# Optimization experiments

Measured on AMD Instinct MI355X. Metric: run time of the kernel, lower is better.

The kernel has to match this reference:

```python
import jax, jax.numpy as jnp
import numpy as np


def setup_inputs() -> dict:
    key = jax.random.key(0)
    ks = jax.random.split(key, 11)
    B, E, R, D = 2048, 20000, 500, 256
    inp = {
        "h": jax.random.uniform(ks[0], (B, E), dtype=jnp.float32),
        "t": jax.random.uniform(ks[1], (B, E), dtype=jnp.float32),
        "r": jax.random.uniform(ks[2], (B, R), dtype=jnp.float32),
        "W_er": jax.random.normal(ks[3], (D, E), dtype=jnp.float32) * 0.02,
        "W_ei": jax.random.normal(ks[4], (D, E), dtype=jnp.float32) * 0.02,
        "W_ej": jax.random.normal(ks[5], (D, E), dtype=jnp.float32) * 0.02,
        "W_ek": jax.random.normal(ks[6], (D, E), dtype=jnp.float32) * 0.02,
        "W_rr": jax.random.normal(ks[7], (D, R), dtype=jnp.float32) * 0.02,
        "W_ri": jax.random.normal(ks[8], (D, R), dtype=jnp.float32) * 0.02,
        "W_rj": jax.random.normal(ks[9], (D, R), dtype=jnp.float32) * 0.02,
        "W_rk": jax.random.normal(ks[10], (D, R), dtype=jnp.float32) * 0.02,
    }
    return inp


def reference(h, t, r, W_er, W_ei, W_ej, W_ek, W_rr, W_ri, W_rj, W_rk):
    # entity / relation projections (nn.Linear, no bias): x @ W^T -> [B, D]
    H_r, H_i, H_j, H_k = h @ W_er.T, h @ W_ei.T, h @ W_ej.T, h @ W_ek.T
    T_r, T_i, T_j, T_k = t @ W_er.T, t @ W_ei.T, t @ W_ej.T, t @ W_ek.T
    R_r, R_i, R_j, R_k = r @ W_rr.T, r @ W_ri.T, r @ W_rj.T, r @ W_rk.T

    # hypercomplex norm per row: sqrt(|R_r|^2 + |R_i|^2 + |R_j|^2 + |R_k|^2) -> [B,1]
    norm = jnp.sqrt(
        jnp.sum(R_r * R_r + R_i * R_i + R_j * R_j + R_k * R_k, axis=1, keepdims=True)
    )
    R_r, R_i, R_j, R_k = norm * R_r, norm * R_i, norm * R_j, norm * R_k

    # Hamilton product H (x) R
    Q_r = H_r * R_r - H_i * R_i - H_j * R_j - H_k * R_k
    Q_i = H_r * R_i + H_i * R_r + H_j * R_k - H_k * R_j
    Q_j = H_r * R_j - H_i * R_k + H_j * R_r + H_k * R_i
    Q_k = H_r * R_k + H_i * R_j - H_j * R_i + H_k * R_r

    # diag(Q @ T^T) == rowwise dot sum(Q*T, axis=1) -- O(B*d) form of the anti-pattern
    score = jnp.sum(Q_r * T_r + Q_i * T_i + Q_j * T_j + Q_k * T_k, axis=1, keepdims=True)
    return jax.nn.sigmoid(score)
```

## Files before the change

### kernel.cpp

```cpp
#include <hip/hip_runtime.h>


using bf16x8 = __attribute__((ext_vector_type(8))) short;
using f32x4  = __attribute__((ext_vector_type(4))) float;

#define DEVINL static __device__ __forceinline__

DEVINL void split2(float x0, float x1, unsigned& h, unsigned& l) {
  unsigned u0 = __float_as_uint(x0), u1 = __float_as_uint(x1);
  unsigned h0 = u0 & 0xFFFF0000u, h1 = u1 & 0xFFFF0000u;
  h = (u0 >> 16) | h1;
  float r0 = x0 - __uint_as_float(h0);
  float r1 = x1 - __uint_as_float(h1);
  l = (__float_as_uint(r0) >> 16) | (__float_as_uint(r1) & 0xFFFF0000u);
}

DEVINL void gload16(const void* g, void* l) {
  __builtin_amdgcn_global_load_lds(
      (const __attribute__((address_space(1))) unsigned*)g,
      (__attribute__((address_space(3))) unsigned*)l, 16, 0, 0);
}

__global__ void convert_b(const float* __restrict__ src, int srcK,
                          char* __restrict__ dst)
{
  const int tile = blockIdx.x;
  const int wrow = threadIdx.x;
  char* base = dst + (size_t)tile * 32768;
  const float* srow = src + (size_t)wrow * srcK;
#pragma unroll
  for (int kc8 = 0; kc8 < 4; ++kc8) {
    int k0 = tile * 32 + kc8 * 8;
    float x[8];
    if (k0 + 8 <= srcK) {
      float4 v0 = *(const float4*)(srow + k0);
      float4 v1 = *(const float4*)(srow + k0 + 4);
      x[0] = v0.x; x[1] = v0.y; x[2] = v0.z; x[3] = v0.w;
      x[4] = v1.x; x[5] = v1.y; x[6] = v1.z; x[7] = v1.w;
    } else {
#pragma unroll
      for (int j = 0; j < 8; ++j) x[j] = (k0 + j < srcK) ? srow[k0 + j] : 0.f;
    }
    unsigned hh[4], ll[4];
    split2(x[0], x[1], hh[0], ll[0]);
    split2(x[2], x[3], hh[1], ll[1]);
    split2(x[4], x[5], hh[2], ll[2]);
    split2(x[6], x[7], hh[3], ll[3]);
    int lchunk = (wrow & 15) + kc8 * 16;
    int n16 = wrow >> 4;
    *(uint4*)(base + (size_t)n16 * 1024 + lchunk * 16)         = make_uint4(hh[0], hh[1], hh[2], hh[3]);
    *(uint4*)(base + 16384 + (size_t)n16 * 1024 + lchunk * 16) = make_uint4(ll[0], ll[1], ll[2], ll[3]);
  }
}

__global__ void pad_r(const float* __restrict__ src, float* __restrict__ dst)
{
  int row = blockIdx.y;
  int c4 = threadIdx.x;
  int k = c4 * 4;
  float4 v = make_float4(0.f, 0.f, 0.f, 0.f);
  if (k + 3 < 500) v = *(const float4*)(src + (size_t)row * 500 + k);
  *(float4*)(dst + (size_t)row * 512 + k) = v;
}

__global__ __launch_bounds__(512, 2) void gemm3p(
    const float* __restrict__ A0, const float* __restrict__ A1, int mtA0, long lda,
    const char* __restrict__ Bimg, int ktilesTot,
    float* __restrict__ C, long ldc, int MT, int NT, int KS, int swz)
{
  extern __shared__ char smem[];
  const int tid = threadIdx.x;
  const int bid = blockIdx.x;

  int mt, nt, ks;
  if (swz) {
    int x = bid & 7, w = bid >> 3;
    nt = w & 3;
    int g = x + (w >> 2) * 8;
    mt = g & 15; ks = g >> 4;
  } else {
    nt = bid % NT; int q = bid / NT; mt = q % MT; ks = q / MT;
  }

  const int kt0 = (ktilesTot * ks) / KS;
  const int kt1 = (ktilesTot * (ks + 1)) / KS;

  const float* Ablk = (mt < mtA0) ? (A0 + (size_t)mt * 256 * lda)
                                  : (A1 + (size_t)(mt - mtA0) * 256 * lda);
  const char* Bt = Bimg + ((size_t)nt * ktilesTot + kt0) * 32768;

  const int wid = tid >> 6, lane = tid & 63;
  const int wr = wid >> 2, wc = wid & 3;
  const int l15 = lane & 15, lq = lane >> 4;

  const float* aSrc = Ablk + (size_t)(wid * 32 + (lane >> 3)) * lda
                      + (size_t)kt0 * 32 + 4 * (lane & 7);

  int awoff[4];
  {
    int kg = (lane & 7) >> 1, half = lane & 1;
#pragma unroll
    for (int i = 0; i < 4; ++i) {
      int m15 = (lane >> 3) + 8 * (i & 1);
      awoff[i] = (2 * wid + (i >> 1)) * 2048 + (((m15 ^ kg) + kg * 16) << 4) + half * 8;
    }
  }
  const int aroff = (((l15 ^ lq) + lq * 16) << 4);
  const int bbase = 32768 + (wc * 4) * 1024 + lane * 16;

  f32x4 acc[8][4];
#pragma unroll
  for (int m = 0; m < 8; ++m)
#pragma unroll
    for (int j = 0; j < 4; ++j)
#pragma unroll
      for (int e = 0; e < 4; ++e) acc[m][j][e] = 0.f;

  float4 aR[4];

#define ISSUE_A(KT)                                                            \
  {                                                                            \
    const float* p_ = aSrc + (size_t)((KT) - kt0) * 32;                        \
    _Pragma("unroll")                                                          \
    for (int i = 0; i < 4; ++i) aR[i] = *(const float4*)(p_ + (size_t)(8 * i) * lda); \
  }
#define ISSUE_B(DST, KT)                                                       \
  {                                                                            \
    const char* p_ = Bt + (size_t)((KT) - kt0) * 32768 + wid * 4096 + lane * 16; \
    _Pragma("unroll")                                                          \
    for (int i = 0; i < 4; ++i)                                                \
      gload16(p_ + i * 1024, (DST) + 32768 + wid * 4096 + i * 1024);           \
  }
#define WRITE_A(DST)                                                           \
  {                                                                            \
    _Pragma("unroll")                                                          \
    for (int i = 0; i < 4; ++i) {                                              \
      unsigned h0_, l0_, h1_, l1_;                                             \
      split2(aR[i].x, aR[i].y, h0_, l0_);                                      \
      split2(aR[i].z, aR[i].w, h1_, l1_);                                      \
      *(uint2*)((DST) + awoff[i])        = make_uint2(h0_, h1_);               \
      *(uint2*)((DST) + awoff[i] + 1024) = make_uint2(l0_, l1_);               \
    }                                                                          \
  }

  ISSUE_A(kt0);
  ISSUE_B(smem, kt0);
  WRITE_A(smem);
  asm volatile("s_waitcnt vmcnt(0)" ::: "memory");
  asm volatile("s_waitcnt lgkmcnt(0)" ::: "memory");
  __builtin_amdgcn_s_barrier();

  for (int kt = kt0; kt < kt1; ++kt) {
    char* bufc = smem + (size_t)((kt - kt0) & 1) * 65536;
    char* bufn = smem + (size_t)(((kt - kt0) & 1) ^ 1) * 65536;
    const bool nx = (kt + 1 < kt1);

    if (nx) { ISSUE_A(kt + 1); ISSUE_B(bufn, kt + 1); }

    bf16x8 bh[4], bl[4];
#pragma unroll
    for (int j = 0; j < 4; ++j) {
      bh[j] = *(const bf16x8*)(bufc + bbase + j * 1024);
      bl[j] = *(const bf16x8*)(bufc + bbase + j * 1024 + 16384);
    }

    __builtin_amdgcn_s_setprio(1);
#pragma unroll
    for (int m = 0; m < 4; ++m) {
      const char* ab = bufc + (wr * 8 + m) * 2048;
      bf16x8 ah = *(const bf16x8*)(ab + aroff);
      bf16x8 al = *(const bf16x8*)(ab + aroff + 1024);
#pragma unroll
      for (int j = 0; j < 4; ++j) {
        acc[m][j] = __builtin_amdgcn_mfma_f32_16x16x32_bf16(ah, bh[j], acc[m][j], 0, 0, 0);
        acc[m][j] = __builtin_amdgcn_mfma_f32_16x16x32_bf16(al, bh[j], acc[m][j], 0, 0, 0);
        acc[m][j] = __builtin_amdgcn_mfma_f32_16x16x32_bf16(ah, bl[j], acc[m][j], 0, 0, 0);
      }
    }
    __builtin_amdgcn_s_setprio(0);

    __builtin_amdgcn_sched_barrier(0);
    if (nx) WRITE_A(bufn);

    __builtin_amdgcn_s_setprio(1);
#pragma unroll
    for (int m = 4; m < 8; ++m) {
      const char* ab = bufc + (wr * 8 + m) * 2048;
      bf16x8 ah = *(const bf16x8*)(ab + aroff);
      bf16x8 al = *(const bf16x8*)(ab + aroff + 1024);
#pragma unroll
      for (int j = 0; j < 4; ++j) {
        acc[m][j] = __builtin_amdgcn_mfma_f32_16x16x32_bf16(ah, bh[j], acc[m][j], 0, 0, 0);
        acc[m][j] = __builtin_amdgcn_mfma_f32_16x16x32_bf16(al, bh[j], acc[m][j], 0, 0, 0);
        acc[m][j] = __builtin_amdgcn_mfma_f32_16x16x32_bf16(ah, bl[j], acc[m][j], 0, 0, 0);
      }
    }
    __builtin_amdgcn_s_setprio(0);

    asm volatile("s_waitcnt vmcnt(0)" ::: "memory");
    asm volatile("s_waitcnt lgkmcnt(0)" ::: "memory");
    __builtin_amdgcn_s_barrier();
  }
#undef ISSUE_A
#undef ISSUE_B
#undef WRITE_A

  float* Cb = C + (size_t)ks * (size_t)(MT * 256) * (size_t)ldc;
  const long rowbase = (long)mt * 256 + wr * 128 + lq * 4;
  const long colbase = (long)nt * 256 + wc * 64 + l15;
#pragma unroll
  for (int m = 0; m < 8; ++m)
#pragma unroll
    for (int j = 0; j < 4; ++j)
#pragma unroll
      for (int reg = 0; reg < 4; ++reg) {
        long row = rowbase + m * 16 + reg;
        long col = colbase + j * 16;
        Cb[(size_t)row * ldc + col] = acc[m][j][reg];
      }
}

__global__ void epilogue_kernel(const float* __restrict__ C1, const float* __restrict__ C2,
                                float* __restrict__ out, int KS)
{
  const int b = blockIdx.x;
  const int d = threadIdx.x;
  const size_t SZ = 4096ull * 1024ull;

  float Hq[4], Tq[4], Rq[4];
#pragma unroll
  for (int q = 0; q < 4; ++q) {
    float hv = 0.f, tv = 0.f;
    for (int ks = 0; ks < KS; ++ks) {
      hv += C1[ks * SZ + (size_t)b * 1024 + q * 256 + d];
      tv += C1[ks * SZ + (size_t)(b + 2048) * 1024 + q * 256 + d];
    }
    Hq[q] = hv; Tq[q] = tv;
    Rq[q] = C2[(size_t)b * 1024 + q * 256 + d];
  }
  float nn = Rq[0]*Rq[0] + Rq[1]*Rq[1] + Rq[2]*Rq[2] + Rq[3]*Rq[3];
  float Qr = Hq[0]*Rq[0] - Hq[1]*Rq[1] - Hq[2]*Rq[2] - Hq[3]*Rq[3];
  float Qi = Hq[0]*Rq[1] + Hq[1]*Rq[0] + Hq[2]*Rq[3] - Hq[3]*Rq[2];
  float Qj = Hq[0]*Rq[2] - Hq[1]*Rq[3] + Hq[2]*Rq[0] + Hq[3]*Rq[1];
  float Qk = Hq[0]*Rq[3] + Hq[1]*Rq[2] - Hq[2]*Rq[1] + Hq[3]*Rq[0];
  float ss = Qr*Tq[0] + Qi*Tq[1] + Qj*Tq[2] + Qk*Tq[3];

#pragma unroll
  for (int o = 32; o; o >>= 1) {
    ss += __shfl_xor(ss, o);
    nn += __shfl_xor(nn, o);
  }
  __shared__ float red[8];
  int lane = d & 63, w = d >> 6;
  if (lane == 0) { red[w] = ss; red[4 + w] = nn; }
  __syncthreads();
  if (d == 0) {
    float S = red[0] + red[1] + red[2] + red[3];
    float N = red[4] + red[5] + red[6] + red[7];
    float score = sqrtf(N) * S;
    out[b] = 1.f / (1.f + expf(-score));
  }
}

extern "C" void kernel_launch(void* const* d_in, const int* in_sizes, int n_in,
                              void* d_out, int out_size, void* d_ws, size_t ws_size,
                              hipStream_t stream)
{
  const float* h = (const float*)d_in[0];
  const float* t = (const float*)d_in[1];
  const float* r = (const float*)d_in[2];
  const float* We[4] = {(const float*)d_in[3], (const float*)d_in[4],
                        (const float*)d_in[5], (const float*)d_in[6]};
  const float* Wr[4] = {(const float*)d_in[7], (const float*)d_in[8],
                        (const float*)d_in[9], (const float*)d_in[10]};
  float* out = (float*)d_out;

  char* ws = (char*)d_ws;
  const size_t offB  = 0;
  const size_t offWr = 81920000;
  const size_t offR  = offWr + 2097152;
  const size_t offC1 = offR + 4194304;
  const size_t C1sz  = 4096ull * 1024ull * 4ull;
  const int KS = (ws_size >= offC1 + 4 * C1sz + 8388608ull) ? 4 : 2;
  const size_t offC2 = offC1 + (size_t)KS * C1sz;

  float* rpad = (float*)(ws + offR);
  float* C1   = (float*)(ws + offC1);
  float* C2   = (float*)(ws + offC2);

  for (int q = 0; q < 4; ++q) {
    convert_b<<<dim3(625), 256, 0, stream>>>(We[q], 20000, ws + offB + (size_t)q * 625 * 32768);
    convert_b<<<dim3(16), 256, 0, stream>>>(Wr[q], 500, ws + offWr + (size_t)q * 16 * 32768);
  }
  pad_r<<<dim3(1, 2048), 128, 0, stream>>>(r, rpad);

  gemm3p<<<dim3(16 * 4 * KS), 512, 131072, stream>>>(
      h, t, 8, 20000L, (const char*)(ws + offB), 625,
      C1, 1024L, 16, 4, KS, KS == 4 ? 1 : 0);
  gemm3p<<<dim3(32), 512, 131072, stream>>>(
      rpad, rpad, 8, 512L, (const char*)(ws + offWr), 16,
      C2, 1024L, 8, 4, 1, 0);

  epilogue_kernel<<<dim3(2048), 256, 0, stream>>>(C1, C2, out, KS);
}
```

Before: 687.2 us.

## Split GEMM main loop into four barrier-synchronized LDS-read/MFMA phases

The per-k-tile inner loop is restructured into four phases, each reading A fragments for two m-rows from LDS and then running their MFMAs, with workgroup barriers between phases. All waves thereby alternate LDS-read and MFMA bursts in lockstep, aiming to cut LDS contention and overlap the global prefetch with compute. The extra barriers add synchronization overhead and can stall waves that would otherwise run ahead, and the final lgkmcnt wait before the loop-end barrier is removed.

```diff
diff --git a/kernel.cpp b/kernel.cpp
--- a/kernel.cpp
+++ b/kernel.cpp
@@ -142,6 +142,33 @@
       *(uint2*)((DST) + awoff[i] + 1024) = make_uint2(l0_, l1_);               \
     }                                                                          \
   }
+#define MFMA_PAIR(M0)                                                          \
+  {                                                                            \
+    _Pragma("unroll")                                                          \
+    for (int mm = 0; mm < 2; ++mm) {                                           \
+      bf16x8 ah = a_h[mm], al = a_l[mm];                                       \
+      _Pragma("unroll")                                                        \
+      for (int j = 0; j < 4; ++j) {                                            \
+        f32x4* a = &acc[(M0) + mm][j];                                         \
+        *a = __builtin_amdgcn_mfma_f32_16x16x32_bf16(ah, bh[j], *a, 0, 0, 0);  \
+        *a = __builtin_amdgcn_mfma_f32_16x16x32_bf16(al, bh[j], *a, 0, 0, 0);  \
+        *a = __builtin_amdgcn_mfma_f32_16x16x32_bf16(ah, bl[j], *a, 0, 0, 0);  \
+      }                                                                        \
+    }                                                                          \
+  }
+#define READ_A_PAIR(M0)                                                        \
+  {                                                                            \
+    _Pragma("unroll")                                                          \
+    for (int mm = 0; mm < 2; ++mm) {                                           \
+      const char* ab_ = abase + ((M0) + mm) * 2048;                            \
+      a_h[mm] = *(const bf16x8*)(ab_ + aroff);                                 \
+      a_l[mm] = *(const bf16x8*)(ab_ + aroff + 1024);                          \
+    }                                                                          \
+  }
+#define PHASE_SYNC()                                                           \
+  __builtin_amdgcn_s_barrier();                                                \
+  asm volatile("s_waitcnt lgkmcnt(0)" ::: "memory");                           \
+  __builtin_amdgcn_sched_barrier(0);
 
   ISSUE_A(kt0);
   ISSUE_B(smem, kt0);
@@ -154,56 +181,52 @@
     char* bufc = smem + (size_t)((kt - kt0) & 1) * 65536;
     char* bufn = smem + (size_t)(((kt - kt0) & 1) ^ 1) * 65536;
     const bool nx = (kt + 1 < kt1);
+    const char* abase = bufc + wr * 8 * 2048;
+
+    bf16x8 bh[4], bl[4], a_h[2], a_l[2];
 
     if (nx) { ISSUE_A(kt + 1); ISSUE_B(bufn, kt + 1); }
-
-    bf16x8 bh[4], bl[4];
 #pragma unroll
     for (int j = 0; j < 4; ++j) {
       bh[j] = *(const bf16x8*)(bufc + bbase + j * 1024);
       bl[j] = *(const bf16x8*)(bufc + bbase + j * 1024 + 16384);
     }
-
+    READ_A_PAIR(0);
+    PHASE_SYNC();
     __builtin_amdgcn_s_setprio(1);
-#pragma unroll
-    for (int m = 0; m < 4; ++m) {
-      const char* ab = bufc + (wr * 8 + m) * 2048;
-      bf16x8 ah = *(const bf16x8*)(ab + aroff);
-      bf16x8 al = *(const bf16x8*)(ab + aroff + 1024);
-#pragma unroll
-      for (int j = 0; j < 4; ++j) {
-        acc[m][j] = __builtin_amdgcn_mfma_f32_16x16x32_bf16(ah, bh[j], acc[m][j], 0, 0, 0);
-        acc[m][j] = __builtin_amdgcn_mfma_f32_16x16x32_bf16(al, bh[j], acc[m][j], 0, 0, 0);
-        acc[m][j] = __builtin_amdgcn_mfma_f32_16x16x32_bf16(ah, bl[j], acc[m][j], 0, 0, 0);
-      }
-    }
+    MFMA_PAIR(0);
     __builtin_amdgcn_s_setprio(0);
-
-    __builtin_amdgcn_sched_barrier(0);
+    __builtin_amdgcn_s_barrier();
+
+    READ_A_PAIR(2);
+    PHASE_SYNC();
+    __builtin_amdgcn_s_setprio(1);
+    MFMA_PAIR(2);
+    __builtin_amdgcn_s_setprio(0);
+    __builtin_amdgcn_s_barrier();
+
     if (nx) WRITE_A(bufn);
-
+    READ_A_PAIR(4);
+    PHASE_SYNC();
     __builtin_amdgcn_s_setprio(1);
-#pragma unroll
-    for (int m = 4; m < 8; ++m) {
-      const char* ab = bufc + (wr * 8 + m) * 2048;
-      bf16x8 ah = *(const bf16x8*)(ab + aroff);
-      bf16x8 al = *(const bf16x8*)(ab + aroff + 1024);
-#pragma unroll
-      for (int j = 0; j < 4; ++j) {
-        acc[m][j] = __builtin_amdgcn_mfma_f32_16x16x32_bf16(ah, bh[j], acc[m][j], 0, 0, 0);
-        acc[m][j] = __builtin_amdgcn_mfma_f32_16x16x32_bf16(al, bh[j], acc[m][j], 0, 0, 0);
-        acc[m][j] = __builtin_amdgcn_mfma_f32_16x16x32_bf16(ah, bl[j], acc[m][j], 0, 0, 0);
-      }
-    }
+    MFMA_PAIR(4);
     __builtin_amdgcn_s_setprio(0);
-
+    __builtin_amdgcn_s_barrier();
+
+    READ_A_PAIR(6);
+    PHASE_SYNC();
+    __builtin_amdgcn_s_setprio(1);
+    MFMA_PAIR(6);
+    __builtin_amdgcn_s_setprio(0);
     asm volatile("s_waitcnt vmcnt(0)" ::: "memory");
-    asm volatile("s_waitcnt lgkmcnt(0)" ::: "memory");
     __builtin_amdgcn_s_barrier();
   }
 #undef ISSUE_A
 #undef ISSUE_B
 #undef WRITE_A
+#undef MFMA_PAIR
+#undef READ_A_PAIR
+#undef PHASE_SYNC
 
   float* Cb = C + (size_t)ks * (size_t)(MT * 256) * (size_t)ldc;
   const long rowbase = (long)mt * 256 + wr * 128 + lq * 4;
```

Result: slower. 739.8 us (+7.7%).

## Pre-split activations into bf16 hi/lo tile images and use 32x32 MFMA GEMM

Applied to the files above, without the earlier changes.

Adds a conversion pass that writes h, t and r as pre-split bf16 hi/lo tiled images, so the GEMM loads both operands straight into LDS with global_load_lds instead of splitting A in registers each k-tile. The new GEMM uses 32x32x16 MFMA with a 4x2 block per wave and a static 128KB shared buffer. This removes per-tile VALU splitting and register staging of A, but adds a full extra pass that reads the large activations and writes an image of the same size. The new path runs only when the workspace is large enough, otherwise it falls back to the old kernels.

```diff
diff --git a/kernel.cpp b/kernel.cpp
--- a/kernel.cpp
+++ b/kernel.cpp
@@ -3,6 +3,7 @@
 
 using bf16x8 = __attribute__((ext_vector_type(8))) short;
 using f32x4  = __attribute__((ext_vector_type(4))) float;
+using f32x16 = __attribute__((ext_vector_type(16))) float;
 
 #define DEVINL static __device__ __forceinline__
 
@@ -21,8 +22,153 @@
       (__attribute__((address_space(3))) unsigned*)l, 16, 0, 0);
 }
 
-__global__ void convert_b(const float* __restrict__ src, int srcK,
-                          char* __restrict__ dst)
+__global__ void convert_img(const float* __restrict__ src0,
+                            const float* __restrict__ src1, int rows0,
+                            int srcK, char* __restrict__ dst, int ktiles)
+{
+  const int kt = blockIdx.x, rt = blockIdx.y;
+  const int m  = threadIdx.x;
+  const int row = rt * 256 + m;
+  const float* srow = (row < rows0) ? (src0 + (size_t)row * srcK)
+                                    : (src1 + (size_t)(row - rows0) * srcK);
+  char* base = dst + ((size_t)rt * ktiles + kt) * 32768
+             + (m >> 5) * 2048 + (m & 31) * 16;
+#pragma unroll
+  for (int oct = 0; oct < 4; ++oct) {
+    int k0 = kt * 32 + oct * 8;
+    float x[8];
+    if (k0 + 8 <= srcK) {
+      float4 v0 = *(const float4*)(srow + k0);
+      float4 v1 = *(const float4*)(srow + k0 + 4);
+      x[0] = v0.x; x[1] = v0.y; x[2] = v0.z; x[3] = v0.w;
+      x[4] = v1.x; x[5] = v1.y; x[6] = v1.z; x[7] = v1.w;
+    } else {
+#pragma unroll
+      for (int j = 0; j < 8; ++j) x[j] = (k0 + j < srcK) ? srow[k0 + j] : 0.f;
+    }
+    unsigned hh[4], ll[4];
+    split2(x[0], x[1], hh[0], ll[0]);
+    split2(x[2], x[3], hh[1], ll[1]);
+    split2(x[4], x[5], hh[2], ll[2]);
+    split2(x[6], x[7], hh[3], ll[3]);
+    int off = (oct >> 1) * 1024 + (oct & 1) * 512;
+    *(uint4*)(base + off)         = make_uint4(hh[0], hh[1], hh[2], hh[3]);
+    *(uint4*)(base + 16384 + off) = make_uint4(ll[0], ll[1], ll[2], ll[3]);
+  }
+}
+
+__global__ __launch_bounds__(512, 2) void gemm_img(
+    const char* __restrict__ Aimg, const char* __restrict__ Bimg, int ktiles,
+    float* __restrict__ C, int MT, int NT, int KS, int swz)
+{
+  __shared__ __align__(16) char smem[131072];
+  const int tid = threadIdx.x;
+  const int bid = blockIdx.x;
+
+  int mt, nt, ks;
+  if (swz) {
+    int x = bid & 7, w = bid >> 3;
+    nt = w & 3;
+    int g = x + (w >> 2) * 8;
+    mt = g & 15; ks = g >> 4;
+  } else {
+    nt = bid % NT; int q = bid / NT; mt = q % MT; ks = q / MT;
+  }
+
+  const int kt0 = (ktiles * ks) / KS;
+  const int kt1 = (ktiles * (ks + 1)) / KS;
+
+  const char* Ab = Aimg + ((size_t)mt * ktiles + kt0) * 32768;
+  const char* Bb = Bimg + ((size_t)nt * ktiles + kt0) * 32768;
+
+  const int wid = tid >> 6, lane = tid & 63;
+  const int wr = wid >> 2, wc = wid & 3;
+
+  f32x16 acc[4][2];
+#pragma unroll
+  for (int mb = 0; mb < 4; ++mb)
+#pragma unroll
+    for (int nb = 0; nb < 2; ++nb)
+#pragma unroll
+      for (int e = 0; e < 16; ++e) acc[mb][nb][e] = 0.f;
+
+  {
+    const char* As = Ab + wid * 4096 + lane * 16;
+    const char* Bs = Bb + wid * 4096 + lane * 16;
+#pragma unroll
+    for (int i = 0; i < 4; ++i) gload16(As + i * 1024, smem + wid * 4096 + i * 1024);
+#pragma unroll
+    for (int i = 0; i < 4; ++i) gload16(Bs + i * 1024, smem + 32768 + wid * 4096 + i * 1024);
+  }
+  asm volatile("s_waitcnt vmcnt(0)" ::: "memory");
+  __builtin_amdgcn_s_barrier();
+
+  for (int kt = kt0; kt < kt1; ++kt) {
+    char* bufc = smem + (size_t)((kt - kt0) & 1) * 65536;
+    char* bufn = smem + (size_t)(((kt - kt0) & 1) ^ 1) * 65536;
+    const bool nx = (kt + 1 < kt1);
+
+    if (nx) {
+      const char* As = Ab + (size_t)(kt + 1 - kt0) * 32768 + wid * 4096 + lane * 16;
+      const char* Bs = Bb + (size_t)(kt + 1 - kt0) * 32768 + wid * 4096 + lane * 16;
+#pragma unroll
+      for (int i = 0; i < 4; ++i) gload16(As + i * 1024, bufn + wid * 4096 + i * 1024);
+#pragma unroll
+      for (int i = 0; i < 4; ++i) gload16(Bs + i * 1024, bufn + 32768 + wid * 4096 + i * 1024);
+    }
+
+    bf16x8 bh[2][2], bl[2][2];
+#pragma unroll
+    for (int nb = 0; nb < 2; ++nb)
+#pragma unroll
+      for (int s = 0; s < 2; ++s) {
+        const char* p = bufc + 32768 + (wc * 2 + nb) * 2048 + s * 1024 + lane * 16;
+        bh[nb][s] = *(const bf16x8*)p;
+        bl[nb][s] = *(const bf16x8*)(p + 16384);
+      }
+
+    __builtin_amdgcn_s_setprio(1);
+#pragma unroll
+    for (int mb = 0; mb < 4; ++mb) {
+      const char* p = bufc + (wr * 4 + mb) * 2048 + lane * 16;
+      bf16x8 ah0 = *(const bf16x8*)(p);
+      bf16x8 al0 = *(const bf16x8*)(p + 16384);
+      bf16x8 ah1 = *(const bf16x8*)(p + 1024);
+      bf16x8 al1 = *(const bf16x8*)(p + 1024 + 16384);
+#pragma unroll
+      for (int nb = 0; nb < 2; ++nb) {
+        f32x16* a = &acc[mb][nb];
+        *a = __builtin_amdgcn_mfma_f32_32x32x16_bf16(ah0, bh[nb][0], *a, 0, 0, 0);
+        *a = __builtin_amdgcn_mfma_f32_32x32x16_bf16(al0, bh[nb][0], *a, 0, 0, 0);
+        *a = __builtin_amdgcn_mfma_f32_32x32x16_bf16(ah0, bl[nb][0], *a, 0, 0, 0);
+        *a = __builtin_amdgcn_mfma_f32_32x32x16_bf16(ah1, bh[nb][1], *a, 0, 0, 0);
+        *a = __builtin_amdgcn_mfma_f32_32x32x16_bf16(al1, bh[nb][1], *a, 0, 0, 0);
+        *a = __builtin_amdgcn_mfma_f32_32x32x16_bf16(ah1, bl[nb][1], *a, 0, 0, 0);
+      }
+    }
+    __builtin_amdgcn_s_setprio(0);
+
+    asm volatile("s_waitcnt vmcnt(0)" ::: "memory");
+    __builtin_amdgcn_s_barrier();
+  }
+
+  float* Cb = C + (size_t)ks * (size_t)(MT * 256) * 1024;
+  const long rowbase = (long)mt * 256 + wr * 128 + 4 * (lane >> 5);
+  const long colbase = (long)nt * 256 + wc * 64 + (lane & 31);
+#pragma unroll
+  for (int mb = 0; mb < 4; ++mb)
+#pragma unroll
+    for (int nb = 0; nb < 2; ++nb)
+#pragma unroll
+      for (int reg = 0; reg < 16; ++reg) {
+        long row = rowbase + mb * 32 + (reg & 3) + 8 * (reg >> 2);
+        long col = colbase + nb * 32;
+        Cb[(size_t)row * 1024 + col] = acc[mb][nb][reg];
+      }
+}
+
+__global__ void convert_b16(const float* __restrict__ src, int srcK,
+                            char* __restrict__ dst)
 {
   const int tile = blockIdx.x;
   const int wrow = threadIdx.x;
@@ -56,8 +202,7 @@
 __global__ void pad_r(const float* __restrict__ src, float* __restrict__ dst)
 {
   int row = blockIdx.y;
-  int c4 = threadIdx.x;
-  int k = c4 * 4;
+  int k = threadIdx.x * 4;
   float4 v = make_float4(0.f, 0.f, 0.f, 0.f);
   if (k + 3 < 500) v = *(const float4*)(src + (size_t)row * 500 + k);
   *(float4*)(dst + (size_t)row * 512 + k) = v;
@@ -68,7 +213,7 @@
     const char* __restrict__ Bimg, int ktilesTot,
     float* __restrict__ C, long ldc, int MT, int NT, int KS, int swz)
 {
-  extern __shared__ char smem[];
+  extern __shared__ char smemd[];
   const int tid = threadIdx.x;
   const int bid = blockIdx.x;
 
@@ -144,15 +289,15 @@
   }
 
   ISSUE_A(kt0);
-  ISSUE_B(smem, kt0);
-  WRITE_A(smem);
+  ISSUE_B(smemd, kt0);
+  WRITE_A(smemd);
   asm volatile("s_waitcnt vmcnt(0)" ::: "memory");
   asm volatile("s_waitcnt lgkmcnt(0)" ::: "memory");
   __builtin_amdgcn_s_barrier();
 
   for (int kt = kt0; kt < kt1; ++kt) {
-    char* bufc = smem + (size_t)((kt - kt0) & 1) * 65536;
-    char* bufn = smem + (size_t)(((kt - kt0) & 1) ^ 1) * 65536;
+    char* bufc = smemd + (size_t)((kt - kt0) & 1) * 65536;
+    char* bufn = smemd + (size_t)(((kt - kt0) & 1) ^ 1) * 65536;
     const bool nx = (kt + 1 < kt1);
 
     if (nx) { ISSUE_A(kt + 1); ISSUE_B(bufn, kt + 1); }
@@ -274,31 +419,61 @@
   const float* Wr[4] = {(const float*)d_in[7], (const float*)d_in[8],
                         (const float*)d_in[9], (const float*)d_in[10]};
   float* out = (float*)d_out;
-
   char* ws = (char*)d_ws;
-  const size_t offB  = 0;
-  const size_t offWr = 81920000;
-  const size_t offR  = offWr + 2097152;
-  const size_t offC1 = offR + 4194304;
+
+  const size_t offA  = 0;
+  const size_t offB  = 327680000;
+  const size_t offWr = offB + 81920000;
+  const size_t offRi = offWr + 2097152;
+  const size_t offC1 = offRi + 4194304;
   const size_t C1sz  = 4096ull * 1024ull * 4ull;
-  const int KS = (ws_size >= offC1 + 4 * C1sz + 8388608ull) ? 4 : 2;
-  const size_t offC2 = offC1 + (size_t)KS * C1sz;
-
-  float* rpad = (float*)(ws + offR);
-  float* C1   = (float*)(ws + offC1);
-  float* C2   = (float*)(ws + offC2);
+  const size_t offC2 = offC1 + 4 * C1sz;
+  const size_t needImg = offC2 + 8388608;
+
+  if (ws_size >= needImg) {
+    float* C1 = (float*)(ws + offC1);
+    float* C2 = (float*)(ws + offC2);
+
+    convert_img<<<dim3(625, 16), 256, 0, stream>>>(h, t, 2048, 20000, ws + offA, 625);
+    for (int q = 0; q < 4; ++q) {
+      convert_img<<<dim3(625, 1), 256, 0, stream>>>(
+          We[q], We[q], 2048, 20000, ws + offB + (size_t)q * 625 * 32768, 625);
+      convert_img<<<dim3(16, 1), 256, 0, stream>>>(
+          Wr[q], Wr[q], 2048, 500, ws + offWr + (size_t)q * 16 * 32768, 16);
+    }
+    convert_img<<<dim3(16, 8), 256, 0, stream>>>(r, r, 4096, 500, ws + offRi, 16);
+
+    gemm_img<<<dim3(256), 512, 0, stream>>>(
+        ws + offA, ws + offB, 625, C1, 16, 4, 4, 1);
+    gemm_img<<<dim3(32), 512, 0, stream>>>(
+        ws + offRi, ws + offWr, 16, C2, 8, 4, 1, 0);
+
+    epilogue_kernel<<<dim3(2048), 256, 0, stream>>>(C1, C2, out, 4);
+    return;
+  }
+
+  const size_t fB  = 0;
+  const size_t fWr = 81920000;
+  const size_t fR  = fWr + 2097152;
+  const size_t fC1 = fR + 4194304;
+  const int KS = (ws_size >= fC1 + 4 * C1sz + 8388608ull) ? 4 : 2;
+  const size_t fC2 = fC1 + (size_t)KS * C1sz;
+
+  float* rpad = (float*)(ws + fR);
+  float* C1   = (float*)(ws + fC1);
+  float* C2   = (float*)(ws + fC2);
 
   for (int q = 0; q < 4; ++q) {
-    convert_b<<<dim3(625), 256, 0, stream>>>(We[q], 20000, ws + offB + (size_t)q * 625 * 32768);
-    convert_b<<<dim3(16), 256, 0, stream>>>(Wr[q], 500, ws + offWr + (size_t)q * 16 * 32768);
+    convert_b16<<<dim3(625), 256, 0, stream>>>(We[q], 20000, ws + fB + (size_t)q * 625 * 32768);
+    convert_b16<<<dim3(16), 256, 0, stream>>>(Wr[q], 500, ws + fWr + (size_t)q * 16 * 32768);
   }
   pad_r<<<dim3(1, 2048), 128, 0, stream>>>(r, rpad);
 
   gemm3p<<<dim3(16 * 4 * KS), 512, 131072, stream>>>(
-      h, t, 8, 20000L, (const char*)(ws + offB), 625,
+      h, t, 8, 20000L, (const char*)(ws + fB), 625,
       C1, 1024L, 16, 4, KS, KS == 4 ? 1 : 0);
   gemm3p<<<dim3(32), 512, 131072, stream>>>(
-      rpad, rpad, 8, 512L, (const char*)(ws + offWr), 16,
+      rpad, rpad, 8, 512L, (const char*)(ws + fWr), 16,
       C2, 1024L, 8, 4, 1, 0);
 
   epilogue_kernel<<<dim3(2048), 256, 0, stream>>>(C1, C2, out, KS);
```

After: 690.1 us. About the same (+0.4%).
